# Kernel tuning notes

Hardware: AMD Instinct MI355X
Metric: run time of the kernel (lower is better)

Reference implementation:

```python
import jax, jax.numpy as jnp
import numpy as np

BS = 512
N_BOXES = 30   # num_boxes*3 in the torch module
K = 15
HID = 128
EMB = 64
FEAT = HID + EMB + 2  # 194


def _knn_idx(x, k):
    # x: (bs, n, 4); per-sample kNN (self excluded), matching pyg knn_graph with batch
    d = jnp.sum((x[:, :, None, :] - x[:, None, :, :]) ** 2, axis=-1)  # (bs, n, n)
    n = x.shape[1]
    d = d + jnp.eye(n, dtype=x.dtype) * 1e9  # exclude self-loops
    _, idx = jax.lax.top_k(-d, k)  # k nearest sources j for each target i
    return idx  # (bs, n, k)


def _edge_conv(x, idx, Wa, ba, Wb, bb):
    # EdgeConv: out_i = max_j mlp([x_i, x_j - x_i]), aggr='max'
    xj = jax.vmap(lambda xb, ib: xb[ib])(x, idx)            # (bs, n, k, F)
    xi = jnp.broadcast_to(x[:, :, None, :], xj.shape)        # (bs, n, k, F)
    m = jnp.concatenate([xi, xj - xi], axis=-1)              # (bs, n, k, 2F)
    h = jax.nn.relu(jnp.einsum('bnkf,hf->bnkh', m, Wa) + ba)
    h = jnp.einsum('bnkh,oh->bnko', h, Wb) + bb
    return jnp.max(h, axis=2)                                # (bs, n, HID)


def _q(nodes, emb, Wi, bi, Wma, bma, Wmb, bmb, Wca, bca, Wcb, bcb):
    bs, n, _ = nodes.shape
    idx = _knn_idx(nodes, K)
    cats = jnp.repeat(jnp.arange(3), n // 3)                 # [0]*10+[1]*10+[2]*10
    cls = jax.nn.relu(emb[cats])                             # (n, EMB)
    cls = jnp.broadcast_to(cls[None], (bs, n, EMB))
    tar = jnp.zeros((bs, n, 2), nodes.dtype)                 # tanh(zeros) = 0
    init = jnp.concatenate([jax.nn.relu(nodes @ Wi.T + bi), cls, tar], axis=-1)
    h = jax.nn.relu(_edge_conv(init, idx, Wma, bma, Wmb, bmb))
    h = jax.nn.relu(h @ Wca.T + bca)
    out = h @ Wcb.T + bcb                                    # (bs, n, 1)
    return out.reshape(bs, -1)


def setup_inputs() -> dict:
    key = jax.random.key(0)
    ks = jax.random.split(key, 22)
    rn = lambda k, shp: (jax.random.normal(k, shp) * 0.05).astype(jnp.float32)
    return {
        'state': jax.random.normal(ks[0], (BS, N_BOXES * 2), jnp.float32),
        'action': jax.random.normal(ks[1], (BS, N_BOXES * 2), jnp.float32),
        'W_init1': rn(ks[2], (HID, 4)), 'b_init1': rn(ks[3], (HID,)),
        'emb1': rn(ks[4], (3, EMB)),
        'W_m1a': rn(ks[5], (HID, 2 * FEAT)), 'b_m1a': rn(ks[6], (HID,)),
        'W_m1b': rn(ks[7], (HID, HID)), 'b_m1b': rn(ks[8], (HID,)),
        'W_c1a': rn(ks[9], (HID, HID)), 'b_c1a': rn(ks[10], (HID,)),
        'W_c1b': rn(ks[11], (1, HID)), 'b_c1b': rn(ks[12], (1,)),
        'W_init2': rn(ks[13], (HID, 4)), 'b_init2': rn(ks[14], (HID,)),
        'emb2': rn(ks[15], (3, EMB)),
        'W_c2a': rn(ks[16], (HID, HID)), 'b_c2a': rn(ks[17], (HID,)),
        'W_c2b': rn(ks[18], (1, HID)), 'b_c2b': rn(ks[19], (1,)),
    }


def reference(state, action, W_init1, b_init1, emb1, W_m1a, b_m1a, W_m1b, b_m1b,
              W_c1a, b_c1a, W_c1b, b_c1b, W_init2, b_init2, emb2,
              W_c2a, b_c2a, W_c2b, b_c2b):
    bs = state.shape[0]
    # Q1 node layout: interleaved per-box [sx, sy, ax, ay]
    nodes1 = jnp.concatenate([state.reshape(bs, N_BOXES, 2),
                              action.reshape(bs, N_BOXES, 2)], axis=-1)
    q1 = _q(nodes1, emb1, W_init1, b_init1, W_m1a, b_m1a, W_m1b, b_m1b,
            W_c1a, b_c1a, W_c1b, b_c1b)
    # Q2 node layout (faithful to torch bug): cat along dim 1 then view(-1, 4)
    nodes2 = jnp.concatenate([state, action], axis=1).reshape(bs, N_BOXES, 4)
    # conv1_2 reuses mlp1_1 weights (faithful to torch source)
    q2 = _q(nodes2, emb2, W_init2, b_init2, W_m1a, b_m1a, W_m1b, b_m1b,
            W_c2a, b_c2a, W_c2b, b_c2b)
    return (q1, q2)
```

## Files before the change

### kernel.cpp

```cpp
#include <hip/hip_runtime.h>

#define BSZ 512
#define NNODE 30
#define KNBR 15
#define HID 128
#define MTOT (BSZ*NNODE)

typedef __attribute__((ext_vector_type(8))) __bf16 bf16x8;
typedef __attribute__((ext_vector_type(4))) float f32x4;

__device__ __forceinline__ float frelu(float x){ return x > 0.f ? x : 0.f; }

__device__ __forceinline__ void node_coords(const float* __restrict__ st,
                                            const float* __restrict__ ac,
                                            int b, int n, int qsel, float c[4]) {
    if (qsel == 0) {
        c[0] = st[b*60 + 2*n];     c[1] = st[b*60 + 2*n + 1];
        c[2] = ac[b*60 + 2*n];     c[3] = ac[b*60 + 2*n + 1];
    } else {
        int base = 4*n;
        if (base < 60) {
            c[0]=st[b*60+base]; c[1]=st[b*60+base+1]; c[2]=st[b*60+base+2]; c[3]=st[b*60+base+3];
        } else {
            int a = base - 60;
            c[0]=ac[b*60+a]; c[1]=ac[b*60+a+1]; c[2]=ac[b*60+a+2]; c[3]=ac[b*60+a+3];
        }
    }
}

__global__ void k_prep(const float* __restrict__ Wa,  const float* __restrict__ Wb,
                       const float* __restrict__ Wca1,const float* __restrict__ Wca2,
                       const float* __restrict__ ba,
                       const float* __restrict__ emb1,const float* __restrict__ emb2,
                       __bf16* __restrict__ Wc16, __bf16* __restrict__ Wb16,
                       __bf16* __restrict__ Wca16_1, __bf16* __restrict__ Wca16_2,
                       float* __restrict__ cls1A, float* __restrict__ cls1B,
                       float* __restrict__ cls2A, float* __restrict__ cls2B) {
    int blk = blockIdx.x;
    if (blk < 320) {
        int t = blk*256 + threadIdx.x;
        if (t < 32768) {
            int o = t >> 7, h = t & 127;
            float v = (o < 128) ? (Wa[o*388 + h] - Wa[o*388 + 194 + h])
                                : Wa[(o-128)*388 + 194 + h];
            Wc16[t] = (__bf16)v;
        } else if (t < 49152) { int u = t - 32768; Wb16[u]    = (__bf16)Wb[u]; }
        else if (t < 65536)   { int u = t - 49152; Wca16_1[u] = (__bf16)Wca1[u]; }
        else                  { int u = t - 65536; Wca16_2[u] = (__bf16)Wca2[u]; }
    } else {
        int o = threadIdx.x;
        if (o >= 128) return;
        const float* emb = (blk == 320) ? emb1  : emb2;
        float* cA        = (blk == 320) ? cls1A : cls2A;
        float* cB        = (blk == 320) ? cls1B : cls2B;
        for (int c = 0; c < 3; ++c) {
            float sA = ba[o], sB = 0.f;
            for (int e = 0; e < 64; ++e) {
                float r  = frelu(emb[c*64 + e]);
                float wl = Wa[o*388 + 128 + e];
                float wr = Wa[o*388 + 194 + 128 + e];
                sA += (wl - wr) * r;
                sB += wr * r;
            }
            cA[c*128 + o] = sA;
            cB[c*128 + o] = sB;
        }
    }
}

__global__ void __launch_bounds__(256, 4) k_fused(
        const float* __restrict__ st, const float* __restrict__ ac,
        const float* __restrict__ Wi1, const float* __restrict__ bi1,
        const float* __restrict__ Wi2, const float* __restrict__ bi2,
        const __bf16* __restrict__ Wc16,
        const float* __restrict__ cls1A, const float* __restrict__ cls1B,
        const float* __restrict__ cls2A, const float* __restrict__ cls2B,
        const __bf16* __restrict__ Wb16, const float* __restrict__ bb,
        const __bf16* __restrict__ Wca16_1, const float* __restrict__ bca1,
        const float* __restrict__ Wcb1, const float* __restrict__ bcb1,
        const __bf16* __restrict__ Wca16_2, const float* __restrict__ bca2,
        const float* __restrict__ Wcb2, const float* __restrict__ bcb2,
        float* __restrict__ out) {
    __shared__ float  coords[30][4];
    __shared__ int    idxs[30*16];
    __shared__ __align__(16) __bf16 Vf[2][4][4][16][8];
    __shared__ __align__(16) __bf16 Al[30*136];
    __shared__ __align__(16) __bf16 Bl[30*136];
    __shared__ __align__(16) __bf16 El[32*136];
    __shared__ float  redh[4][16];

    int tid  = threadIdx.x;
    int lane = tid & 63, wid = tid >> 6;
    int l15  = lane & 15, g = (lane >> 4) & 3;
    int bid  = blockIdx.x;
    int q    = bid >> 9, b = bid & 511;

    const float* Wi   = q ? Wi2 : Wi1;
    const float* bi   = q ? bi2 : bi1;
    const float* clsA = q ? cls2A : cls1A;
    const float* clsB = q ? cls2B : cls1B;
    const __bf16* Wca16 = q ? Wca16_2 : Wca16_1;
    const float* bca  = q ? bca2 : bca1;
    const float* Wcb  = q ? Wcb2 : Wcb1;
    const float* bcb  = q ? bcb2 : bcb1;

    if (tid < 30) {
        float c[4]; node_coords(st, ac, b, tid, q, c);
        coords[tid][0]=c[0]; coords[tid][1]=c[1]; coords[tid][2]=c[2]; coords[tid][3]=c[3];
    }
    __syncthreads();

    if (tid < 30) {
        int i = tid;
        float ci0=coords[i][0], ci1=coords[i][1], ci2=coords[i][2], ci3=coords[i][3];
        float d[30];
        #pragma unroll
        for (int j = 0; j < 30; ++j) {
            float d0 = ci0-coords[j][0], d1 = ci1-coords[j][1];
            float d2 = ci2-coords[j][2], d3 = ci3-coords[j][3];
            d[j] = d0*d0 + d1*d1 + d2*d2 + d3*d3;
        }
        unsigned mask = 1u << i;
        for (int k = 0; k < KNBR; ++k) {
            float best = 3.4e38f; int bj = 0;
            #pragma unroll
            for (int j = 0; j < 30; ++j) {
                bool ok = !((mask >> j) & 1u) && (d[j] < best);
                if (ok) { best = d[j]; bj = j; }
            }
            mask |= 1u << bj;
            idxs[i*16 + k] = bj;
        }
        idxs[i*16 + 15] = idxs[i*16];
    } else if (tid >= 32) {
        for (int e = tid - 32; e < 4096; e += 224) {
            int m = e >> 7, h = e & 127;
            float v = 0.f;
            if (m < 30) {
                v = frelu(bi[h] + Wi[h*4+0]*coords[m][0] + Wi[h*4+1]*coords[m][1]
                                + Wi[h*4+2]*coords[m][2] + Wi[h*4+3]*coords[m][3]);
            }
            Vf[m>>4][h>>5][(h>>3)&3][m&15][h&7] = (__bf16)v;
        }
    }
    if (tid >= 30 && tid < 32) { }
    __syncthreads();

    {
        int mt = wid & 1, half = wid >> 1;
        bf16x8 af[4];
        #pragma unroll
        for (int kk = 0; kk < 4; ++kk) af[kk] = *(const bf16x8*)&Vf[mt][kk][g][l15][0];
        f32x4 acc[8];
        #pragma unroll
        for (int nc = 0; nc < 8; ++nc) acc[nc] = (f32x4){0.f,0.f,0.f,0.f};
        #pragma unroll
        for (int nc = 0; nc < 8; ++nc) {
            int o256 = half*128 + nc*16 + l15;
            bf16x8 wf[4];
            #pragma unroll
            for (int kk = 0; kk < 4; ++kk)
                wf[kk] = *(const bf16x8*)(Wc16 + o256*128 + kk*32 + g*8);
            #pragma unroll
            for (int kk = 0; kk < 4; ++kk)
                acc[nc] = __builtin_amdgcn_mfma_f32_16x16x32_bf16(af[kk], wf[kk], acc[nc], 0, 0, 0);
        }
        const float* cls = half ? clsB : clsA;
        __bf16* dst = half ? Bl : Al;
        #pragma unroll
        for (int nc = 0; nc < 8; ++nc) {
            #pragma unroll
            for (int r = 0; r < 4; ++r) {
                int m = mt*16 + g*4 + r;
                if (m < 30) {
                    int o = nc*16 + l15;
                    int cat = m / 10;
                    dst[m*136 + o] = (__bf16)(acc[nc][r] + cls[cat*128 + o]);
                }
            }
        }
    }
    __syncthreads();

    {
        for (int ch = 0; ch < 2; ++ch) {
            bf16x8 wbf[4][4];
            #pragma unroll
            for (int oc = 0; oc < 4; ++oc)
                #pragma unroll
                for (int kk = 0; kk < 4; ++kk)
                    wbf[oc][kk] = *(const bf16x8*)(Wb16 + ((ch*4+oc)*16 + l15)*128 + kk*32 + g*8);
            float bbv[4];
            #pragma unroll
            for (int oc = 0; oc < 4; ++oc) bbv[oc] = bb[(ch*4+oc)*16 + l15];

            for (int i = wid; i < 30; i += 4) {
                int nb = idxs[i*16 + l15];
                bf16x8 hf[4];
                #pragma unroll
                for (int kk = 0; kk < 4; ++kk) {
                    bf16x8 pa = *(const bf16x8*)&Al[i*136  + kk*32 + g*8];
                    bf16x8 pb = *(const bf16x8*)&Bl[nb*136 + kk*32 + g*8];
                    bf16x8 h;
                    #pragma unroll
                    for (int e = 0; e < 8; ++e)
                        h[e] = (__bf16)frelu((float)pa[e] + (float)pb[e]);
                    hf[kk] = h;
                }
                f32x4 acc[4];
                #pragma unroll
                for (int oc = 0; oc < 4; ++oc) acc[oc] = (f32x4){0.f,0.f,0.f,0.f};
                #pragma unroll
                for (int kk = 0; kk < 4; ++kk)
                    #pragma unroll
                    for (int oc = 0; oc < 4; ++oc)
                        acc[oc] = __builtin_amdgcn_mfma_f32_16x16x32_bf16(hf[kk], wbf[oc][kk], acc[oc], 0, 0, 0);
                #pragma unroll
                for (int oc = 0; oc < 4; ++oc) {
                    float v = fmaxf(fmaxf(acc[oc][0], acc[oc][1]), fmaxf(acc[oc][2], acc[oc][3]));
                    v = fmaxf(v, __shfl_xor(v, 16));
                    v = fmaxf(v, __shfl_xor(v, 32));
                    if (g == 0) El[i*136 + (ch*4+oc)*16 + l15] = (__bf16)frelu(v + bbv[oc]);
                }
            }
        }
        if (tid < 136) ((unsigned*)El)[2040 + tid] = 0u;
    }
    __syncthreads();

    {
        int mt = wid & 1, half = wid >> 1;
        bf16x8 ef[4];
        #pragma unroll
        for (int kk = 0; kk < 4; ++kk)
            ef[kk] = *(const bf16x8*)&El[(mt*16 + l15)*136 + kk*32 + g*8];
        float s[4] = {0.f, 0.f, 0.f, 0.f};
        #pragma unroll
        for (int nc = 0; nc < 4; ++nc) {
            int o = half*64 + nc*16 + l15;
            bf16x8 wf[4];
            #pragma unroll
            for (int kk = 0; kk < 4; ++kk)
                wf[kk] = *(const bf16x8*)(Wca16 + o*128 + kk*32 + g*8);
            f32x4 a = (f32x4){0.f,0.f,0.f,0.f};
            #pragma unroll
            for (int kk = 0; kk < 4; ++kk)
                a = __builtin_amdgcn_mfma_f32_16x16x32_bf16(ef[kk], wf[kk], a, 0, 0, 0);
            float bcav = bca[o], wcbv = Wcb[o];
            #pragma unroll
            for (int r = 0; r < 4; ++r) s[r] += frelu(a[r] + bcav) * wcbv;
        }
        #pragma unroll
        for (int r = 0; r < 4; ++r) {
            s[r] += __shfl_xor(s[r], 1);
            s[r] += __shfl_xor(s[r], 2);
            s[r] += __shfl_xor(s[r], 4);
            s[r] += __shfl_xor(s[r], 8);
        }
        if (l15 == 0) {
            #pragma unroll
            for (int r = 0; r < 4; ++r) redh[wid][g*4 + r] = s[r];
        }
    }
    __syncthreads();
    if (tid < 30) {
        int mt = tid >> 4, mr = tid & 15;
        out[q*MTOT + b*30 + tid] = redh[mt][mr] + redh[mt+2][mr] + bcb[0];
    }
}

extern "C" void kernel_launch(void* const* d_in, const int* in_sizes, int n_in,
                              void* d_out, int out_size, void* d_ws, size_t ws_size,
                              hipStream_t stream) {
    const float* state  = (const float*)d_in[0];
    const float* action = (const float*)d_in[1];
    const float* W_init1= (const float*)d_in[2];
    const float* b_init1= (const float*)d_in[3];
    const float* emb1   = (const float*)d_in[4];
    const float* W_m1a  = (const float*)d_in[5];
    const float* b_m1a  = (const float*)d_in[6];
    const float* W_m1b  = (const float*)d_in[7];
    const float* b_m1b  = (const float*)d_in[8];
    const float* W_c1a  = (const float*)d_in[9];
    const float* b_c1a  = (const float*)d_in[10];
    const float* W_c1b  = (const float*)d_in[11];
    const float* b_c1b  = (const float*)d_in[12];
    const float* W_init2= (const float*)d_in[13];
    const float* b_init2= (const float*)d_in[14];
    const float* emb2   = (const float*)d_in[15];
    const float* W_c2a  = (const float*)d_in[16];
    const float* b_c2a  = (const float*)d_in[17];
    const float* W_c2b  = (const float*)d_in[18];
    const float* b_c2b  = (const float*)d_in[19];

    __bf16* Wc16    = (__bf16*)d_ws;
    __bf16* Wb16    = Wc16 + 32768;
    __bf16* Wca16_1 = Wb16 + 16384;
    __bf16* Wca16_2 = Wca16_1 + 16384;
    float*  cls1A   = (float*)(Wca16_2 + 16384);
    float*  cls1B   = cls1A + 384;
    float*  cls2A   = cls1B + 384;
    float*  cls2B   = cls2A + 384;
    float*  out     = (float*)d_out;

    k_prep<<<322, 256, 0, stream>>>(W_m1a, W_m1b, W_c1a, W_c2a, b_m1a, emb1, emb2,
                                    Wc16, Wb16, Wca16_1, Wca16_2,
                                    cls1A, cls1B, cls2A, cls2B);

    k_fused<<<2*BSZ, 256, 0, stream>>>(state, action,
                                       W_init1, b_init1, W_init2, b_init2,
                                       Wc16, cls1A, cls1B, cls2A, cls2B,
                                       Wb16, b_m1b,
                                       Wca16_1, b_c1a, W_c1b, b_c1b,
                                       Wca16_2, b_c2a, W_c2b, b_c2b,
                                       out);
}
```

Baseline: 173.7 us.

## Alias shared buffers into one arena, raise occupancy bound, vectorize init feature writes

Replaces the separate shared arrays with one byte arena where the Vf/El and coords/redh buffers overlap because their lifetimes do not. This cuts LDS per block so more blocks can be resident, and the launch bound hint goes from 4 to 8 blocks per CU. The init-feature loop now has each thread compute 8 consecutive hidden units and store them as a single 16-byte bf16x8 write instead of scalar bf16 stores. The tighter register budget from the higher bound may cause spills, and the aliasing relies on correct barrier ordering between phases.

```diff
diff --git a/kernel.cpp b/kernel.cpp
--- a/kernel.cpp
+++ b/kernel.cpp
@@ -68,7 +68,7 @@
     }
 }
 
-__global__ void __launch_bounds__(256, 4) k_fused(
+__global__ void __launch_bounds__(256, 8) k_fused(
         const float* __restrict__ st, const float* __restrict__ ac,
         const float* __restrict__ Wi1, const float* __restrict__ bi1,
         const float* __restrict__ Wi2, const float* __restrict__ bi2,
@@ -81,13 +81,14 @@
         const __bf16* __restrict__ Wca16_2, const float* __restrict__ bca2,
         const float* __restrict__ Wcb2, const float* __restrict__ bcb2,
         float* __restrict__ out) {
-    __shared__ float  coords[30][4];
-    __shared__ int    idxs[30*16];
-    __shared__ __align__(16) __bf16 Vf[2][4][4][16][8];
-    __shared__ __align__(16) __bf16 Al[30*136];
-    __shared__ __align__(16) __bf16 Bl[30*136];
-    __shared__ __align__(16) __bf16 El[32*136];
-    __shared__ float  redh[4][16];
+    __shared__ __align__(16) char smem[27424];
+    __bf16 (*Vf)[4][4][16][8] = reinterpret_cast<__bf16 (*)[4][4][16][8]>(smem);
+    __bf16* El   = (__bf16*)smem;
+    __bf16* Al   = (__bf16*)(smem + 8704);
+    __bf16* Bl   = (__bf16*)(smem + 16864);
+    int*    idxs = (int*)(smem + 25024);
+    float (*coords)[4] = (float(*)[4])(smem + 26944);
+    float (*redh)[16]  = (float(*)[16])(smem + 26944);
 
     int tid  = threadIdx.x;
     int lane = tid & 63, wid = tid >> 6;
@@ -133,17 +134,25 @@
         }
         idxs[i*16 + 15] = idxs[i*16];
     } else if (tid >= 32) {
-        for (int e = tid - 32; e < 4096; e += 224) {
-            int m = e >> 7, h = e & 127;
-            float v = 0.f;
+        for (int it = tid - 32; it < 512; it += 224) {
+            int row = it & 15, g2 = (it >> 4) & 3, kk2 = (it >> 6) & 3, mt2 = it >> 8;
+            int m = mt2*16 + row;
+            bf16x8 v8;
             if (m < 30) {
-                v = frelu(bi[h] + Wi[h*4+0]*coords[m][0] + Wi[h*4+1]*coords[m][1]
-                                + Wi[h*4+2]*coords[m][2] + Wi[h*4+3]*coords[m][3]);
-            }
-            Vf[m>>4][h>>5][(h>>3)&3][m&15][h&7] = (__bf16)v;
-        }
-    }
-    if (tid >= 30 && tid < 32) { }
+                float c0=coords[m][0], c1=coords[m][1], c2=coords[m][2], c3=coords[m][3];
+                #pragma unroll
+                for (int e = 0; e < 8; ++e) {
+                    int h = kk2*32 + g2*8 + e;
+                    v8[e] = (__bf16)frelu(bi[h] + Wi[h*4+0]*c0 + Wi[h*4+1]*c1
+                                                + Wi[h*4+2]*c2 + Wi[h*4+3]*c3);
+                }
+            } else {
+                #pragma unroll
+                for (int e = 0; e < 8; ++e) v8[e] = (__bf16)0.f;
+            }
+            *(bf16x8*)&Vf[mt2][kk2][g2][row][0] = v8;
+        }
+    }
     __syncthreads();
 
     {
```

Result: slower. 191.7 us (+10.3%).
